# Performance work log

Hardware: AMD Instinct MI355X
Metric: run time of the kernel (lower is better)

## Reference

```python
import jax, jax.numpy as jnp
import numpy as np

NP, NQ, E, D = 100000, 50000, 600000, 128


def _seg_mean(x, idx, n):
    # mean aggregation per destination node (PyG scatter-mean, zero for isolated nodes)
    s = jax.ops.segment_sum(x, idx, num_segments=n)
    c = jax.ops.segment_sum(jnp.ones((idx.shape[0], 1), x.dtype), idx, num_segments=n)
    return s / jnp.maximum(c, 1.0)


def setup_inputs() -> dict:
    key = jax.random.key(0)
    ks = jax.random.split(key, 20)
    sc = 1.0 / np.sqrt(D)
    inp = {
        'x_person': jax.random.normal(ks[0], (NP, D), jnp.float32),
        'x_product': jax.random.normal(ks[1], (NQ, D), jnp.float32),
        'src_pv': jax.random.randint(ks[2], (E,), 0, NP, jnp.int32),
        'dst_pv': jax.random.randint(ks[3], (E,), 0, NQ, jnp.int32),
        'src_vp': jax.random.randint(ks[4], (E,), 0, NQ, jnp.int32),
        'dst_vp': jax.random.randint(ks[5], (E,), 0, NP, jnp.int32),
    }
    i = 6
    for layer in (0, 1):
        for et in ('pv', 'vp'):
            inp[f'Wl_{et}{layer}'] = jax.random.normal(ks[i], (D, D), jnp.float32) * sc; i += 1
            inp[f'Wr_{et}{layer}'] = jax.random.normal(ks[i], (D, D), jnp.float32) * sc; i += 1
            inp[f'b_{et}{layer}'] = jnp.zeros((D,), jnp.float32)
    return inp


def _layer(h_p, h_q, src_pv, dst_pv, src_vp, dst_vp, Wl_pv, Wr_pv, b_pv, Wl_vp, Wr_vp, b_vp):
    # SAGEConv per edge type: lin_l(mean_j x_src) + lin_r(x_dst) + bias; HeteroConv aggr='sum'
    agg_q = _seg_mean(h_p[src_pv], dst_pv, NQ)   # person -> product
    agg_p = _seg_mean(h_q[src_vp], dst_vp, NP)   # product -> person
    new_q = agg_q @ Wl_pv + h_q @ Wr_pv + b_pv
    new_p = agg_p @ Wl_vp + h_p @ Wr_vp + b_vp
    return new_p, new_q


def reference(x_person, x_product,
              Wl_pv0, Wr_pv0, b_pv0, Wl_vp0, Wr_vp0, b_vp0,
              Wl_pv1, Wr_pv1, b_pv1, Wl_vp1, Wr_vp1, b_vp1,
              src_pv, dst_pv, src_vp, dst_vp):
    h_p, h_q = _layer(x_person, x_product, src_pv, dst_pv, src_vp, dst_vp,
                      Wl_pv0, Wr_pv0, b_pv0, Wl_vp0, Wr_vp0, b_vp0)
    h_p, h_q = jax.nn.relu(h_p), jax.nn.relu(h_q)  # dropout identity (eval mode)
    h_p, h_q = _layer(h_p, h_q, src_pv, dst_pv, src_vp, dst_vp,
                      Wl_pv1, Wr_pv1, b_pv1, Wl_vp1, Wr_vp1, b_vp1)
    return h_p, h_q
```

## Files before the change

### kernel.cpp

```cpp
#include <hip/hip_runtime.h>

#define D 128
#define PAD 40
#define NBT 256
#define DNMAX 512
#define GT 32
#define GCAP 4096

typedef __attribute__((ext_vector_type(8))) short short8;
typedef __attribute__((ext_vector_type(4))) float f32x4;

__device__ __forceinline__ unsigned short f2bf(float x) {
    union { float f; unsigned u; } v; v.f = x;
    unsigned r = v.u + 0x7fff + ((v.u >> 16) & 1);
    return (unsigned short)(r >> 16);
}

__global__ __launch_bounds__(256) void bhist(const int* __restrict__ dst_pv,
                                             const int* __restrict__ dst_vp, int E,
                                             int shq, int shp,
                                             int* __restrict__ bq, int* __restrict__ bp) {
    __shared__ int hq[NBT], hp[NBT];
    int tid = threadIdx.x;
    if (tid < NBT) { hq[tid] = 0; hp[tid] = 0; }
    __syncthreads();
    for (int e = blockIdx.x * 256 + tid; e < E; e += gridDim.x * 256) {
        atomicAdd(&hq[dst_pv[e] >> shq], 1);
        atomicAdd(&hp[dst_vp[e] >> shp], 1);
    }
    __syncthreads();
    if (tid < NBT) {
        if (hq[tid]) atomicAdd(&bq[tid], hq[tid]);
        if (hp[tid]) atomicAdd(&bp[tid], hp[tid]);
    }
}

__global__ __launch_bounds__(128) void bscan(int* __restrict__ bq, int nbq,
                                             int* __restrict__ bp, int nbp,
                                             int* __restrict__ curq, int* __restrict__ curp,
                                             int* __restrict__ rp_q, int nq,
                                             int* __restrict__ rp_p, int np, int E) {
    int wid = threadIdx.x >> 6, lane = threadIdx.x & 63;
    int* seg = wid ? bp : bq;
    int* cur = wid ? curp : curq;
    int nseg = wid ? nbp : nbq;
    int carry = 0;
    for (int base = 0; base < nseg; base += 64) {
        int i = base + lane;
        int v = (i < nseg) ? seg[i] : 0;
        int inc = v;
        #pragma unroll
        for (int off = 1; off < 64; off <<= 1) {
            int t = __shfl_up(inc, off, 64);
            if (lane >= off) inc += t;
        }
        if (i < nseg) { int ex = carry + inc - v; seg[i] = ex; cur[i] = ex; }
        carry += __shfl(inc, 63, 64);
    }
    if (lane == 0) { if (wid == 0) rp_q[nq] = E; else rp_p[np] = E; }
}

__global__ __launch_bounds__(256) void bscatter(const int* __restrict__ src_pv,
                                                const int* __restrict__ dst_pv,
                                                const int* __restrict__ src_vp,
                                                const int* __restrict__ dst_vp, int E,
                                                int* __restrict__ curq, int shq,
                                                int* __restrict__ curp, int shp,
                                                int2* __restrict__ pairs_q,
                                                int2* __restrict__ pairs_p) {
    __shared__ int cq[NBT], baq[NBT], wq[NBT];
    __shared__ int cp_[NBT], bap[NBT], wp_[NBT];
    int tid = threadIdx.x;
    int nblk = gridDim.x;
    int chunk = (E + nblk - 1) / nblk;
    int lo = blockIdx.x * chunk;
    int hi = min(lo + chunk, E);
    if (tid < NBT) { cq[tid] = 0; cp_[tid] = 0; }
    __syncthreads();
    for (int e = lo + tid; e < hi; e += 256) {
        atomicAdd(&cq[dst_pv[e] >> shq], 1);
        atomicAdd(&cp_[dst_vp[e] >> shp], 1);
    }
    __syncthreads();
    if (tid < NBT) {
        baq[tid] = cq[tid]  ? atomicAdd(&curq[tid], cq[tid])  : 0; wq[tid]  = 0;
        bap[tid] = cp_[tid] ? atomicAdd(&curp[tid], cp_[tid]) : 0; wp_[tid] = 0;
    }
    __syncthreads();
    for (int e = lo + tid; e < hi; e += 256) {
        int d = dst_pv[e]; int b = d >> shq;
        int off = atomicAdd(&wq[b], 1);
        pairs_q[baq[b] + off] = make_int2(src_pv[e], d);
        d = dst_vp[e]; b = d >> shp;
        off = atomicAdd(&wp_[b], 1);
        pairs_p[bap[b] + off] = make_int2(src_vp[e], d);
    }
}

__global__ __launch_bounds__(256) void bcsr(const int2* __restrict__ pairs_q,
                                            const int2* __restrict__ pairs_p,
                                            const int* __restrict__ bbq, int nbq,
                                            const int* __restrict__ bbp, int nbp,
                                            int* __restrict__ rp_q, int nq, int shq,
                                            int* __restrict__ rp_p, int np, int shp,
                                            int* __restrict__ col_q, int* __restrict__ col_p,
                                            int E) {
    int b = blockIdx.x;
    const int2* pairs; const int* bb; int* rp; int* colg; int nb, n, sh;
    if (b < nbq) { pairs = pairs_q; bb = bbq; rp = rp_q; colg = col_q; nb = nbq; n = nq; sh = shq; }
    else { b -= nbq; pairs = pairs_p; bb = bbp; rp = rp_p; colg = col_p; nb = nbp; n = np; sh = shp; }
    int base = bb[b];
    int next = (b + 1 < nb) ? bb[b + 1] : E;
    int cnt = next - base;
    int dlo = b << sh;
    int dn  = min(1 << sh, n - dlo);

    __shared__ int deg[DNMAX];
    __shared__ int cur[DNMAX];
    __shared__ int wsum[4];
    int tid = threadIdx.x, lane = tid & 63, wid = tid >> 6;

    for (int i = tid; i < dn; i += 256) deg[i] = 0;
    __syncthreads();
    for (int i = tid; i < cnt; i += 256)
        atomicAdd(&deg[pairs[base + i].y - dlo], 1);
    __syncthreads();

    int t2 = tid * 2;
    int d0 = (t2 < dn) ? deg[t2] : 0;
    int d1 = (t2 + 1 < dn) ? deg[t2 + 1] : 0;
    int s = d0 + d1;
    int inc = s;
    #pragma unroll
    for (int off = 1; off < 64; off <<= 1) {
        int t = __shfl_up(inc, off, 64);
        if (lane >= off) inc += t;
    }
    if (lane == 63) wsum[wid] = inc;
    __syncthreads();
    int wpre = 0;
    for (int w2 = 0; w2 < wid; ++w2) wpre += wsum[w2];
    int ex = wpre + inc - s;
    if (t2 < dn)     { cur[t2] = ex;           rp[dlo + t2] = base + ex; }
    if (t2 + 1 < dn) { cur[t2 + 1] = ex + d0;  rp[dlo + t2 + 1] = base + ex + d0; }
    __syncthreads();

    for (int i = tid; i < cnt; i += 256) {
        int2 e = pairs[base + i];
        int off = atomicAdd(&cur[e.y - dlo], 1);
        colg[base + off] = e.x;
    }
}

__global__ __launch_bounds__(256) void prep(const float* W0, const float* W1,
                                            const float* W2, const float* W3,
                                            const float* W4, const float* W5,
                                            const float* W6, const float* W7,
                                            unsigned short* __restrict__ wt,
                                            int* __restrict__ bzero,
                                            const float* __restrict__ xp,
                                            unsigned short* __restrict__ xbp, int np4,
                                            const float* __restrict__ xq,
                                            unsigned short* __restrict__ xbq, int nq4) {
    int blk = blockIdx.x;
    int tid = threadIdx.x;
    if (blk < 64) {
        int m = blk >> 3;
        int c0 = (blk & 7) * 16;
        const float* W;
        switch (m) {
            case 0: W = W0; break; case 1: W = W1; break;
            case 2: W = W2; break; case 3: W = W3; break;
            case 4: W = W4; break; case 5: W = W5; break;
            case 6: W = W6; break; default: W = W7; break;
        }
        unsigned short* hi = wt + (size_t)m * 32768;
        unsigned short* lo = hi + 16384;

        __shared__ unsigned short his[16][136];
        __shared__ unsigned short los[16][136];
        int cc = tid & 15;
        int kk = tid >> 4;
        #pragma unroll
        for (int g = 0; g < 8; ++g) {
            int k = g * 16 + kk;
            float x = W[k * 128 + c0 + cc];
            unsigned short h = f2bf(x);
            union { float f; unsigned u; } hv; hv.u = ((unsigned)h) << 16;
            his[cc][k] = h;
            los[cc][k] = f2bf(x - hv.f);
        }
        __syncthreads();
        int cidx = tid >> 4;
        int k8   = (tid & 15) * 8;
        int c = c0 + cidx;
        uint4 vh, vl;
        #pragma unroll
        for (int j = 0; j < 4; ++j) {
            ((unsigned*)&vh)[j] = *(const unsigned*)&his[cidx][k8 + j * 2];
            ((unsigned*)&vl)[j] = *(const unsigned*)&los[cidx][k8 + j * 2];
        }
        *(uint4*)(hi + (size_t)c * 128 + k8) = vh;
        *(uint4*)(lo + (size_t)c * 128 + k8) = vl;
    } else if (blk == 64) {
        for (int i = tid; i < 2 * NBT; i += 256) bzero[i] = 0;
    } else {
        int tot = np4 + nq4;
        int stride = (gridDim.x - 65) * 256;
        for (int g = (blk - 65) * 256 + tid; g < tot; g += stride) {
            const float* src; unsigned short* dst; int i;
            if (g < np4) { src = xp; dst = xbp; i = g; }
            else         { src = xq; dst = xbq; i = g - np4; }
            float4 v = ((const float4*)src)[i];
            ushort4 o;
            o.x = f2bf(v.x); o.y = f2bf(v.y); o.z = f2bf(v.z); o.w = f2bf(v.w);
            ((ushort4*)dst)[i] = o;
        }
    }
}

__global__ __launch_bounds__(256) void agg_all(
    const int* __restrict__ rp_q, const int* __restrict__ col_q,
    const unsigned short* __restrict__ srcq, unsigned short* __restrict__ outq, int nq,
    const int* __restrict__ rp_p, const int* __restrict__ col_p,
    const unsigned short* __restrict__ srcp, unsigned short* __restrict__ outp, int np,
    int ntq) {
    __shared__ int rps[GT + 1];
    __shared__ int cols[GCAP];

    int blk = blockIdx.x;
    const int* rp; const int* col; const unsigned short* src; unsigned short* out; int n, d0;
    if (blk < ntq) { rp = rp_q; col = col_q; src = srcq; out = outq; n = nq; d0 = blk * GT; }
    else { rp = rp_p; col = col_p; src = srcp; out = outp; n = np; d0 = (blk - ntq) * GT; }

    int tid = threadIdx.x;
    int nrow = min(GT, n - d0);
    if (tid <= nrow) rps[tid] = rp[d0 + tid];
    __syncthreads();
    int beg0 = rps[0];
    int cnt = rps[nrow] - beg0;
    bool useLds = cnt <= GCAP;
    if (useLds)
        for (int i = tid; i < cnt; i += 256) cols[i] = col[beg0 + i];
    __syncthreads();

    int wid = tid >> 6, lane = tid & 63;
    int sub = lane >> 4;
    int ch  = lane & 15;

    for (int r = wid; r < nrow; r += 4) {
        int beg = rps[r], end = rps[r + 1];
        float a0 = 0.f, a1 = 0.f, a2 = 0.f, a3 = 0.f;
        float a4 = 0.f, a5 = 0.f, a6 = 0.f, a7 = 0.f;
        for (int i = beg; i < end; i += 8) {
            #pragma unroll
            for (int h2 = 0; h2 < 2; ++h2) {
                int j = i + h2 * 4 + sub;
                if (j < end) {
                    int s = useLds ? cols[j - beg0] : col[j];
                    uint4 v = *(const uint4*)(src + (size_t)s * D + ch * 8);
                    union { unsigned u; float f; } t;
                    t.u = v.x << 16;         a0 += t.f;
                    t.u = v.x & 0xffff0000u; a1 += t.f;
                    t.u = v.y << 16;         a2 += t.f;
                    t.u = v.y & 0xffff0000u; a3 += t.f;
                    t.u = v.z << 16;         a4 += t.f;
                    t.u = v.z & 0xffff0000u; a5 += t.f;
                    t.u = v.w << 16;         a6 += t.f;
                    t.u = v.w & 0xffff0000u; a7 += t.f;
                }
            }
        }
        #pragma unroll
        for (int off = 16; off <= 32; off <<= 1) {
            a0 += __shfl_xor(a0, off); a1 += __shfl_xor(a1, off);
            a2 += __shfl_xor(a2, off); a3 += __shfl_xor(a3, off);
            a4 += __shfl_xor(a4, off); a5 += __shfl_xor(a5, off);
            a6 += __shfl_xor(a6, off); a7 += __shfl_xor(a7, off);
        }
        int deg = end - beg;
        float inv = (deg > 0) ? 1.0f / (float)deg : 0.f;
        if (sub == 0) {
            uint4 o;
            o.x = (unsigned)f2bf(a0 * inv) | ((unsigned)f2bf(a1 * inv) << 16);
            o.y = (unsigned)f2bf(a2 * inv) | ((unsigned)f2bf(a3 * inv) << 16);
            o.z = (unsigned)f2bf(a4 * inv) | ((unsigned)f2bf(a5 * inv) << 16);
            o.w = (unsigned)f2bf(a6 * inv) | ((unsigned)f2bf(a7 * inv) << 16);
            *(uint4*)(out + (size_t)(d0 + r) * D + ch * 8) = o;
        }
    }
}

struct GemmSide {
    const unsigned short* A1;
    const unsigned short* A2;
    const unsigned short* Wt1;
    const unsigned short* Wt2;
    const float* bias;
    float* out;
    unsigned short* hb;
    int n;
};

template <bool RELU, bool WHB>
__device__ __forceinline__ void gemm_body(const GemmSide& S, int bidx) {
    __shared__ unsigned short As[128][PAD];
    __shared__ unsigned short Ws_hi[128][PAD];
    __shared__ unsigned short Ws_lo[128][PAD];

    const int tid  = threadIdx.x;
    const int lane = tid & 63;
    const int w    = tid >> 6;
    const int m0   = bidx * 128;
    const int n    = S.n;

    f32x4 acc[2][8];
    #pragma unroll
    for (int i = 0; i < 2; ++i)
        #pragma unroll
        for (int j = 0; j < 8; ++j) acc[i][j] = (f32x4)0.f;

    const int srow  = tid >> 1;
    const int skoff = (tid & 1) * 16;

    for (int ks = 0; ks < 8; ++ks) {
        const int half = ks >> 2;
        const int kb   = (ks & 3) * 32;
        const unsigned short* A  = half ? S.A2 : S.A1;
        const unsigned short* Wt = half ? S.Wt2 : S.Wt1;

        {
            int grow = m0 + srow;
            if (grow >= n) grow = n - 1;
            const uint4* pa = (const uint4*)(A + (size_t)grow * D + kb + skoff);
            ((uint4*)&As[srow][skoff])[0] = pa[0];
            ((uint4*)&As[srow][skoff])[1] = pa[1];
        }
        {
            const uint4* ph = (const uint4*)(Wt + (size_t)srow * D + kb + skoff);
            ((uint4*)&Ws_hi[srow][skoff])[0] = ph[0];
            ((uint4*)&Ws_hi[srow][skoff])[1] = ph[1];
            const uint4* pl = (const uint4*)(Wt + 16384 + (size_t)srow * D + kb + skoff);
            ((uint4*)&Ws_lo[srow][skoff])[0] = pl[0];
            ((uint4*)&Ws_lo[srow][skoff])[1] = pl[1];
        }
        __syncthreads();

        const int r0 = w * 32;
        const int k8 = (lane >> 4) * 8;
        const int li = lane & 15;

        short8 ah[2];
        #pragma unroll
        for (int m = 0; m < 2; ++m)
            ah[m] = *(const short8*)&As[r0 + m * 16 + li][k8];
        #pragma unroll
        for (int nb = 0; nb < 8; ++nb) {
            int cc = nb * 16 + li;
            short8 bh = *(const short8*)&Ws_hi[cc][k8];
            short8 bl = *(const short8*)&Ws_lo[cc][k8];
            #pragma unroll
            for (int m = 0; m < 2; ++m) {
                acc[m][nb] = __builtin_amdgcn_mfma_f32_16x16x32_bf16(ah[m], bh, acc[m][nb], 0, 0, 0);
                acc[m][nb] = __builtin_amdgcn_mfma_f32_16x16x32_bf16(ah[m], bl, acc[m][nb], 0, 0, 0);
            }
        }
        __syncthreads();
    }

    const int li = lane & 15;
    const int rq = (lane >> 4) * 4;
    float bv[8];
    #pragma unroll
    for (int nb = 0; nb < 8; ++nb) bv[nb] = S.bias[nb * 16 + li];

    #pragma unroll
    for (int m = 0; m < 2; ++m) {
        #pragma unroll
        for (int nb = 0; nb < 8; ++nb) {
            #pragma unroll
            for (int r = 0; r < 4; ++r) {
                int R = m0 + w * 32 + m * 16 + rq + r;
                if (R < n) {
                    int C = nb * 16 + li;
                    float v = acc[m][nb][r] + bv[nb];
                    if (RELU) v = fmaxf(v, 0.f);
                    S.out[(size_t)R * D + C] = v;
                    if (WHB) S.hb[(size_t)R * D + C] = f2bf(v);
                }
            }
        }
    }
}

template <bool RELU, bool WHB>
__global__ __launch_bounds__(256) void gemm_both(GemmSide Sq, GemmSide Sp, int mq) {
    if ((int)blockIdx.x < mq) gemm_body<RELU, WHB>(Sq, blockIdx.x);
    else                      gemm_body<RELU, WHB>(Sp, blockIdx.x - mq);
}

extern "C" void kernel_launch(void* const* d_in, const int* in_sizes, int n_in,
                              void* d_out, int out_size, void* d_ws, size_t ws_size,
                              hipStream_t stream) {
    const float* x_p = (const float*)d_in[0];
    const float* x_q = (const float*)d_in[1];
    const int* src_pv = (const int*)d_in[2];
    const int* dst_pv = (const int*)d_in[3];
    const int* src_vp = (const int*)d_in[4];
    const int* dst_vp = (const int*)d_in[5];
    const float* Wl_pv0 = (const float*)d_in[6];
    const float* Wr_pv0 = (const float*)d_in[7];
    const float* b_pv0  = (const float*)d_in[8];
    const float* Wl_vp0 = (const float*)d_in[9];
    const float* Wr_vp0 = (const float*)d_in[10];
    const float* b_vp0  = (const float*)d_in[11];
    const float* Wl_pv1 = (const float*)d_in[12];
    const float* Wr_pv1 = (const float*)d_in[13];
    const float* b_pv1  = (const float*)d_in[14];
    const float* Wl_vp1 = (const float*)d_in[15];
    const float* Wr_vp1 = (const float*)d_in[16];
    const float* b_vp1  = (const float*)d_in[17];

    const int NP = in_sizes[0] / D;
    const int NQ = in_sizes[1] / D;
    const int E  = in_sizes[2];

    float* out_p = (float*)d_out;
    float* out_q = out_p + (size_t)NP * D;

    int shq = 6; while ((((NQ - 1) >> shq) + 1) > NBT) ++shq;
    int shp = 6; while ((((NP - 1) >> shp) + 1) > NBT) ++shp;
    int nbq = ((NQ - 1) >> shq) + 1;
    int nbp = ((NP - 1) >> shp) + 1;

    char* ws = (char*)d_ws;
    int* rp_q  = (int*)ws;
    int* rp_p  = rp_q + (NQ + 1);
    int* col_q = rp_p + (NP + 1);
    int* col_p = col_q + E;
    int* bq    = col_p + E;
    int* bp    = bq + NBT;
    int* curq  = bp + NBT;
    int* curp  = curq + NBT;
    size_t int_bytes = ((size_t)(NQ + 1) + (NP + 1) + 2 * (size_t)E + 4 * NBT) * sizeof(int);
    int_bytes = (int_bytes + 511) & ~(size_t)511;
    unsigned short* wt = (unsigned short*)(ws + int_bytes);
    size_t wt_bytes = ((size_t)8 * 32768 * sizeof(unsigned short) + 511) & ~(size_t)511;
    unsigned short* xb_p = (unsigned short*)(ws + int_bytes + wt_bytes);
    unsigned short* xb_q = xb_p + (size_t)NP * D;
    unsigned short* hb_p = xb_p;
    unsigned short* hb_q = xb_q;
    unsigned short* aggb_q = xb_q + (size_t)NQ * D;
    unsigned short* aggb_p = aggb_q + (size_t)NQ * D;
    int2* pairs_q = (int2*)aggb_q;
    int2* pairs_p = pairs_q + E;

    prep<<<65 + 2048, 256, 0, stream>>>(Wl_pv0, Wr_pv0, Wl_vp0, Wr_vp0,
                                        Wl_pv1, Wr_pv1, Wl_vp1, Wr_vp1, wt,
                                        bq, x_p, xb_p, NP * D / 4, x_q, xb_q, NQ * D / 4);

    bhist<<<256, 256, 0, stream>>>(dst_pv, dst_vp, E, shq, shp, bq, bp);
    bscan<<<1, 128, 0, stream>>>(bq, nbq, bp, nbp, curq, curp, rp_q, NQ, rp_p, NP, E);
    bscatter<<<512, 256, 0, stream>>>(src_pv, dst_pv, src_vp, dst_vp, E,
                                      curq, shq, curp, shp, pairs_q, pairs_p);
    bcsr<<<nbq + nbp, 256, 0, stream>>>(pairs_q, pairs_p, bq, nbq, bp, nbp,
                                        rp_q, NQ, shq, rp_p, NP, shp, col_q, col_p, E);

    int ntq = (NQ + GT - 1) / GT, ntp = (NP + GT - 1) / GT;
    int mq = (NQ + 127) / 128, mp = (NP + 127) / 128;

    GemmSide Sq0 = { aggb_q, xb_q, wt + 0 * 32768, wt + 1 * 32768, b_pv0, out_q, hb_q, NQ };
    GemmSide Sp0 = { aggb_p, xb_p, wt + 2 * 32768, wt + 3 * 32768, b_vp0, out_p, hb_p, NP };
    GemmSide Sq1 = { aggb_q, hb_q, wt + 4 * 32768, wt + 5 * 32768, b_pv1, out_q, nullptr, NQ };
    GemmSide Sp1 = { aggb_p, hb_p, wt + 6 * 32768, wt + 7 * 32768, b_vp1, out_p, nullptr, NP };

    agg_all<<<ntq + ntp, 256, 0, stream>>>(rp_q, col_q, xb_p, aggb_q, NQ,
                                           rp_p, col_p, xb_q, aggb_p, NP, ntq);
    gemm_both<true, true><<<mq + mp, 256, 0, stream>>>(Sq0, Sp0, mq);

    agg_all<<<ntq + ntp, 256, 0, stream>>>(rp_q, col_q, hb_p, aggb_q, NQ,
                                           rp_p, col_p, hb_q, aggb_p, NP, ntq);
    gemm_both<false, false><<<mq + mp, 256, 0, stream>>>(Sq1, Sp1, mq);
}
```

Measured before the change: 266.7 us.

## Fuse histogram into prep, pack edge pairs, widen gather batch, skip dead fp32 write

Merges the bucket histogram into the weight/feature prep kernel, zeroing the counters with a memset instead. Packs each (src, dst-offset) edge pair into one 32-bit word so the scatter and CSR-build passes move half the bytes. Raises the aggregation gather from 8 to 16 loads in flight per iteration to expose more memory-level parallelism. Stops layer 0 from writing its fp32 output, which layer 1 overwrites anyway; packing assumes src << shift fits in 32 bits.

```diff
diff --git a/kernel.cpp b/kernel.cpp
--- a/kernel.cpp
+++ b/kernel.cpp
@@ -16,22 +16,79 @@
     return (unsigned short)(r >> 16);
 }
 
-__global__ __launch_bounds__(256) void bhist(const int* __restrict__ dst_pv,
-                                             const int* __restrict__ dst_vp, int E,
-                                             int shq, int shp,
-                                             int* __restrict__ bq, int* __restrict__ bp) {
-    __shared__ int hq[NBT], hp[NBT];
+__global__ __launch_bounds__(256) void prep_hist(
+    const float* W0, const float* W1, const float* W2, const float* W3,
+    const float* W4, const float* W5, const float* W6, const float* W7,
+    unsigned short* __restrict__ wt,
+    const int* __restrict__ dst_pv, const int* __restrict__ dst_vp, int E,
+    int shq, int shp, int* __restrict__ bq, int* __restrict__ bp,
+    const float* __restrict__ xp, unsigned short* __restrict__ xbp, int np4,
+    const float* __restrict__ xq, unsigned short* __restrict__ xbq, int nq4) {
+    int blk = blockIdx.x;
     int tid = threadIdx.x;
-    if (tid < NBT) { hq[tid] = 0; hp[tid] = 0; }
-    __syncthreads();
-    for (int e = blockIdx.x * 256 + tid; e < E; e += gridDim.x * 256) {
-        atomicAdd(&hq[dst_pv[e] >> shq], 1);
-        atomicAdd(&hp[dst_vp[e] >> shp], 1);
-    }
-    __syncthreads();
-    if (tid < NBT) {
-        if (hq[tid]) atomicAdd(&bq[tid], hq[tid]);
-        if (hp[tid]) atomicAdd(&bp[tid], hp[tid]);
+    if (blk < 64) {
+        int m = blk >> 3;
+        int c0 = (blk & 7) * 16;
+        const float* W;
+        switch (m) {
+            case 0: W = W0; break; case 1: W = W1; break;
+            case 2: W = W2; break; case 3: W = W3; break;
+            case 4: W = W4; break; case 5: W = W5; break;
+            case 6: W = W6; break; default: W = W7; break;
+        }
+        unsigned short* hi = wt + (size_t)m * 32768;
+        unsigned short* lo = hi + 16384;
+
+        __shared__ unsigned short his[16][136];
+        __shared__ unsigned short los[16][136];
+        int cc = tid & 15;
+        int kk = tid >> 4;
+        #pragma unroll
+        for (int g = 0; g < 8; ++g) {
+            int k = g * 16 + kk;
+            float x = W[k * 128 + c0 + cc];
+            unsigned short h = f2bf(x);
+            union { float f; unsigned u; } hv; hv.u = ((unsigned)h) << 16;
+            his[cc][k] = h;
+            los[cc][k] = f2bf(x - hv.f);
+        }
+        __syncthreads();
+        int cidx = tid >> 4;
+        int k8   = (tid & 15) * 8;
+        int c = c0 + cidx;
+        uint4 vh, vl;
+        #pragma unroll
+        for (int j = 0; j < 4; ++j) {
+            ((unsigned*)&vh)[j] = *(const unsigned*)&his[cidx][k8 + j * 2];
+            ((unsigned*)&vl)[j] = *(const unsigned*)&los[cidx][k8 + j * 2];
+        }
+        *(uint4*)(hi + (size_t)c * 128 + k8) = vh;
+        *(uint4*)(lo + (size_t)c * 128 + k8) = vl;
+    } else if (blk < 320) {
+        __shared__ int hq[NBT], hp[NBT];
+        if (tid < NBT) { hq[tid] = 0; hp[tid] = 0; }
+        __syncthreads();
+        for (int e = (blk - 64) * 256 + tid; e < E; e += 256 * 256) {
+            atomicAdd(&hq[dst_pv[e] >> shq], 1);
+            atomicAdd(&hp[dst_vp[e] >> shp], 1);
+        }
+        __syncthreads();
+        if (tid < NBT) {
+            if (hq[tid]) atomicAdd(&bq[tid], hq[tid]);
+            if (hp[tid]) atomicAdd(&bp[tid], hp[tid]);
+        }
+    } else {
+        int tot = np4 + nq4;
+        int stride = (gridDim.x - 320) * 256;
+        for (int g = (blk - 320) * 256 + tid; g < tot; g += stride) {
+            const float* src; unsigned short* dst; int i;
+            if (g < np4) { src = xp; dst = xbp; i = g; }
+            else         { src = xq; dst = xbq; i = g - np4; }
+            float4 v = ((const float4*)src)[i];
+            ushort4 o;
+            o.x = f2bf(v.x); o.y = f2bf(v.y); o.z = f2bf(v.z); o.w = f2bf(v.w);
+            ((ushort4*)dst)[i] = o;
+        }
     }
 }
 
@@ -66,8 +123,8 @@
                                                 const int* __restrict__ dst_vp, int E,
                                                 int* __restrict__ curq, int shq,
                                                 int* __restrict__ curp, int shp,
-                                                int2* __restrict__ pairs_q,
-                                                int2* __restrict__ pairs_p) {
+                                                unsigned* __restrict__ pk_q,
+                                                unsigned* __restrict__ pk_p) {
     __shared__ int cq[NBT], baq[NBT], wq[NBT];
     __shared__ int cp_[NBT], bap[NBT], wp_[NBT];
     int tid = threadIdx.x;
@@ -75,6 +132,7 @@
     int chunk = (E + nblk - 1) / nblk;
     int lo = blockIdx.x * chunk;
     int hi = min(lo + chunk, E);
+    unsigned mkq = (1u << shq) - 1, mkp = (1u << shp) - 1;
     if (tid < NBT) { cq[tid] = 0; cp_[tid] = 0; }
     __syncthreads();
     for (int e = lo + tid; e < hi; e += 256) {
@@ -90,15 +148,15 @@
     for (int e = lo + tid; e < hi; e += 256) {
         int d = dst_pv[e]; int b = d >> shq;
         int off = atomicAdd(&wq[b], 1);
-        pairs_q[baq[b] + off] = make_int2(src_pv[e], d);
+        pk_q[baq[b] + off] = ((unsigned)src_pv[e] << shq) | ((unsigned)d & mkq);
         d = dst_vp[e]; b = d >> shp;
         off = atomicAdd(&wp_[b], 1);
-        pairs_p[bap[b] + off] = make_int2(src_vp[e], d);
-    }
-}
-
-__global__ __launch_bounds__(256) void bcsr(const int2* __restrict__ pairs_q,
-                                            const int2* __restrict__ pairs_p,
+        pk_p[bap[b] + off] = ((unsigned)src_vp[e] << shp) | ((unsigned)d & mkp);
+    }
+}
+
+__global__ __launch_bounds__(256) void bcsr(const unsigned* __restrict__ pk_q,
+                                            const unsigned* __restrict__ pk_p,
                                             const int* __restrict__ bbq, int nbq,
                                             const int* __restrict__ bbp, int nbp,
                                             int* __restrict__ rp_q, int nq, int shq,
@@ -106,14 +164,15 @@
                                             int* __restrict__ col_q, int* __restrict__ col_p,
                                             int E) {
     int b = blockIdx.x;
-    const int2* pairs; const int* bb; int* rp; int* colg; int nb, n, sh;
-    if (b < nbq) { pairs = pairs_q; bb = bbq; rp = rp_q; colg = col_q; nb = nbq; n = nq; sh = shq; }
-    else { b -= nbq; pairs = pairs_p; bb = bbp; rp = rp_p; colg = col_p; nb = nbp; n = np; sh = shp; }
+    const unsigned* pk; const int* bb; int* rp; int* colg; int nb, n, sh;
+    if (b < nbq) { pk = pk_q; bb = bbq; rp = rp_q; colg = col_q; nb = nbq; n = nq; sh = shq; }
+    else { b -= nbq; pk = pk_p; bb = bbp; rp = rp_p; colg = col_p; nb = nbp; n = np; sh = shp; }
     int base = bb[b];
     int next = (b + 1 < nb) ? bb[b + 1] : E;
     int cnt = next - base;
     int dlo = b << sh;
     int dn  = min(1 << sh, n - dlo);
+    unsigned mask = (1u << sh) - 1;
 
     __shared__ int deg[DNMAX];
     __shared__ int cur[DNMAX];
@@ -123,7 +182,7 @@
     for (int i = tid; i < dn; i += 256) deg[i] = 0;
     __syncthreads();
     for (int i = tid; i < cnt; i += 256)
-        atomicAdd(&deg[pairs[base + i].y - dlo], 1);
+        atomicAdd(&deg[pk[base + i] & mask], 1);
     __syncthreads();
 
     int t2 = tid * 2;
@@ -146,76 +205,9 @@
     __syncthreads();
 
     for (int i = tid; i < cnt; i += 256) {
-        int2 e = pairs[base + i];
-        int off = atomicAdd(&cur[e.y - dlo], 1);
-        colg[base + off] = e.x;
-    }
-}
-
-__global__ __launch_bounds__(256) void prep(const float* W0, const float* W1,
-                                            const float* W2, const float* W3,
-                                            const float* W4, const float* W5,
-                                            const float* W6, const float* W7,
-                                            unsigned short* __restrict__ wt,
-                                            int* __restrict__ bzero,
-                                            const float* __restrict__ xp,
-                                            unsigned short* __restrict__ xbp, int np4,
-                                            const float* __restrict__ xq,
-                                            unsigned short* __restrict__ xbq, int nq4) {
-    int blk = blockIdx.x;
-    int tid = threadIdx.x;
-    if (blk < 64) {
-        int m = blk >> 3;
-        int c0 = (blk & 7) * 16;
-        const float* W;
-        switch (m) {
-            case 0: W = W0; break; case 1: W = W1; break;
-            case 2: W = W2; break; case 3: W = W3; break;
-            case 4: W = W4; break; case 5: W = W5; break;
-            case 6: W = W6; break; default: W = W7; break;
-        }
-        unsigned short* hi = wt + (size_t)m * 32768;
-        unsigned short* lo = hi + 16384;
-
-        __shared__ unsigned short his[16][136];
-        __shared__ unsigned short los[16][136];
-        int cc = tid & 15;
-        int kk = tid >> 4;
-        #pragma unroll
-        for (int g = 0; g < 8; ++g) {
-            int k = g * 16 + kk;
-            float x = W[k * 128 + c0 + cc];
-            unsigned short h = f2bf(x);
-            union { float f; unsigned u; } hv; hv.u = ((unsigned)h) << 16;
-            his[cc][k] = h;
-            los[cc][k] = f2bf(x - hv.f);
-        }
-        __syncthreads();
-        int cidx = tid >> 4;
-        int k8   = (tid & 15) * 8;
-        int c = c0 + cidx;
-        uint4 vh, vl;
-        #pragma unroll
-        for (int j = 0; j < 4; ++j) {
-            ((unsigned*)&vh)[j] = *(const unsigned*)&his[cidx][k8 + j * 2];
-            ((unsigned*)&vl)[j] = *(const unsigned*)&los[cidx][k8 + j * 2];
-        }
-        *(uint4*)(hi + (size_t)c * 128 + k8) = vh;
-        *(uint4*)(lo + (size_t)c * 128 + k8) = vl;
-    } else if (blk == 64) {
-        for (int i = tid; i < 2 * NBT; i += 256) bzero[i] = 0;
-    } else {
-        int tot = np4 + nq4;
-        int stride = (gridDim.x - 65) * 256;
-        for (int g = (blk - 65) * 256 + tid; g < tot; g += stride) {
-            const float* src; unsigned short* dst; int i;
-            if (g < np4) { src = xp; dst = xbp; i = g; }
-            else         { src = xq; dst = xbq; i = g - np4; }
-            float4 v = ((const float4*)src)[i];
-            ushort4 o;
-            o.x = f2bf(v.x); o.y = f2bf(v.y); o.z = f2bf(v.z); o.w = f2bf(v.w);
-            ((ushort4*)dst)[i] = o;
-        }
+        unsigned v = pk[base + i];
+        int off = atomicAdd(&cur[v & mask], 1);
+        colg[base + off] = (int)(v >> sh);
     }
 }
 
@@ -252,22 +244,29 @@
         int beg = rps[r], end = rps[r + 1];
         float a0 = 0.f, a1 = 0.f, a2 = 0.f, a3 = 0.f;
         float a4 = 0.f, a5 = 0.f, a6 = 0.f, a7 = 0.f;
-        for (int i = beg; i < end; i += 8) {
+        for (int i = beg; i < end; i += 16) {
+            uint4 v[4]; bool act[4];
             #pragma unroll
-            for (int h2 = 0; h2 < 2; ++h2) {
+            for (int h2 = 0; h2 < 4; ++h2) {
                 int j = i + h2 * 4 + sub;
-                if (j < end) {
+                act[h2] = j < end;
+                if (act[h2]) {
                     int s = useLds ? cols[j - beg0] : col[j];
-                    uint4 v = *(const uint4*)(src + (size_t)s * D + ch * 8);
+                    v[h2] = *(const uint4*)(src + (size_t)s * D + ch * 8);
+                }
+            }
+            #pragma unroll
+            for (int h2 = 0; h2 < 4; ++h2) {
+                if (act[h2]) {
                     union { unsigned u; float f; } t;
-                    t.u = v.x << 16;         a0 += t.f;
-                    t.u = v.x & 0xffff0000u; a1 += t.f;
-                    t.u = v.y << 16;         a2 += t.f;
-                    t.u = v.y & 0xffff0000u; a3 += t.f;
-                    t.u = v.z << 16;         a4 += t.f;
-                    t.u = v.z & 0xffff0000u; a5 += t.f;
-                    t.u = v.w << 16;         a6 += t.f;
-                    t.u = v.w & 0xffff0000u; a7 += t.f;
+                    t.u = v[h2].x << 16;         a0 += t.f;
+                    t.u = v[h2].x & 0xffff0000u; a1 += t.f;
+                    t.u = v[h2].y << 16;         a2 += t.f;
+                    t.u = v[h2].y & 0xffff0000u; a3 += t.f;
+                    t.u = v[h2].z << 16;         a4 += t.f;
+                    t.u = v[h2].z & 0xffff0000u; a5 += t.f;
+                    t.u = v[h2].w << 16;         a6 += t.f;
+                    t.u = v[h2].w & 0xffff0000u; a7 += t.f;
                 }
             }
         }
@@ -302,7 +301,7 @@
     int n;
 };
 
-template <bool RELU, bool WHB>
+template <bool RELU, bool WF32, bool WHB>
 __device__ __forceinline__ void gemm_body(const GemmSide& S, int bidx) {
     __shared__ unsigned short As[128][PAD];
     __shared__ unsigned short Ws_hi[128][PAD];
@@ -385,18 +384,18 @@
                     int C = nb * 16 + li;
                     float v = acc[m][nb][r] + bv[nb];
                     if (RELU) v = fmaxf(v, 0.f);
-                    S.out[(size_t)R * D + C] = v;
-                    if (WHB) S.hb[(size_t)R * D + C] = f2bf(v);
+                    if (WF32) S.out[(size_t)R * D + C] = v;
+                    if (WHB)  S.hb[(size_t)R * D + C] = f2bf(v);
                 }
             }
         }
     }
 }
 
-template <bool RELU, bool WHB>
+template <bool RELU, bool WF32, bool WHB>
 __global__ __launch_bounds__(256) void gemm_both(GemmSide Sq, GemmSide Sp, int mq) {
-    if ((int)blockIdx.x < mq) gemm_body<RELU, WHB>(Sq, blockIdx.x);
-    else                      gemm_body<RELU, WHB>(Sp, blockIdx.x - mq);
+    if ((int)blockIdx.x < mq) gemm_body<RELU, WF32, WHB>(Sq, blockIdx.x);
+    else                      gemm_body<RELU, WF32, WHB>(Sp, blockIdx.x - mq);
 }
 
 extern "C" void kernel_launch(void* const* d_in, const int* in_sizes, int n_in,
@@ -452,18 +451,19 @@
     unsigned short* hb_q = xb_q;
     unsigned short* aggb_q = xb_q + (size_t)NQ * D;
     unsigned short* aggb_p = aggb_q + (size_t)NQ * D;
-    int2* pairs_q = (int2*)aggb_q;
-    int2* pairs_p = pairs_q + E;
-
-    prep<<<65 + 2048, 256, 0, stream>>>(Wl_pv0, Wr_pv0, Wl_vp0, Wr_vp0,
-                                        Wl_pv1, Wr_pv1, Wl_vp1, Wr_vp1, wt,
-                                        bq, x_p, xb_p, NP * D / 4, x_q, xb_q, NQ * D / 4);
-
-    bhist<<<256, 256, 0, stream>>>(dst_pv, dst_vp, E, shq, shp, bq, bp);
+    unsigned* pk_q = (unsigned*)aggb_q;
+    unsigned* pk_p = pk_q + E;
+
+    hipMemsetAsync(bq, 0, 2 * NBT * sizeof(int), stream);
+    prep_hist<<<320 + 2048, 256, 0, stream>>>(Wl_pv0, Wr_pv0, Wl_vp0, Wr_vp0,
+                                              Wl_pv1, Wr_pv1, Wl_vp1, Wr_vp1, wt,
+                                              dst_pv, dst_vp, E, shq, shp, bq, bp,
+                                              x_p, xb_p, NP * D / 4, x_q, xb_q, NQ * D / 4);
+
     bscan<<<1, 128, 0, stream>>>(bq, nbq, bp, nbp, curq, curp, rp_q, NQ, rp_p, NP, E);
     bscatter<<<512, 256, 0, stream>>>(src_pv, dst_pv, src_vp, dst_vp, E,
-                                      curq, shq, curp, shp, pairs_q, pairs_p);
-    bcsr<<<nbq + nbp, 256, 0, stream>>>(pairs_q, pairs_p, bq, nbq, bp, nbp,
+                                      curq, shq, curp, shp, pk_q, pk_p);
+    bcsr<<<nbq + nbp, 256, 0, stream>>>(pk_q, pk_p, bq, nbq, bp, nbp,
                                         rp_q, NQ, shq, rp_p, NP, shp, col_q, col_p, E);
 
     int ntq = (NQ + GT - 1) / GT, ntp = (NP + GT - 1) / GT;
@@ -476,9 +476,9 @@
 
     agg_all<<<ntq + ntp, 256, 0, stream>>>(rp_q, col_q, xb_p, aggb_q, NQ,
                                            rp_p, col_p, xb_q, aggb_p, NP, ntq);
-    gemm_both<true, true><<<mq + mp, 256, 0, stream>>>(Sq0, Sp0, mq);
+    gemm_both<true, false, true><<<mq + mp, 256, 0, stream>>>(Sq0, Sp0, mq);
 
     agg_all<<<ntq + ntp, 256, 0, stream>>>(rp_q, col_q, hb_p, aggb_q, NQ,
                                            rp_p, col_p, hb_q, aggb_p, NP, ntq);
-    gemm_both<false, false><<<mq + mp, 256, 0, stream>>>(Sq1, Sp1, mq);
-}
+    gemm_both<false, true, false><<<mq + mp, 256, 0, stream>>>(Sq1, Sp1, mq);
+}
```

New measurement: 251.6 us. -5.7%, faster.
